# Kernel optimization log

Measured on AMD Instinct MI355X. Metric: run time of the kernel, lower is better.

The kernel has to match this reference:

```python
import jax, jax.numpy as jnp
import numpy as np

HID = 1024
DEPTH = 2

def _rhn_layer(x, Win, bin_, Wh, bh, Wt, bt):
    # x: [B, T, in]; returns outputs [B, T, H]
    B = x.shape[0]
    h0 = jnp.zeros((B, HID), dtype=x.dtype)
    xt = jnp.swapaxes(x, 0, 1)  # [T, B, in]

    def step(h_prev, x_t):
        h = x_t @ Win + bin_
        for i in range(DEPTH):
            t_gate = jax.nn.sigmoid(h @ Wt[i] + bt[i])
            h_layer = jnp.tanh(h @ Wh[i] + bh[i])
            h = t_gate * h_layer + (1.0 - t_gate) * h
        h_new = h + h_prev
        return h_new, h_new

    _, outs = jax.lax.scan(step, h0, xt)  # [T, B, H]
    return jnp.swapaxes(outs, 0, 1)


def setup_inputs() -> dict:
    key = jax.random.key(0)
    ks = jax.random.split(key, 16)
    B, T, IN, H, OUT = 64, 256, 128, HID, 128
    s = lambda fan_in: 1.0 / np.sqrt(fan_in)
    d = {}
    d["x"] = jax.random.normal(ks[0], (B, T, IN), dtype=jnp.float32)
    # layer 0 (input_size=IN)
    d["l0_Win"] = jax.random.uniform(ks[1], (IN, H), minval=-s(IN), maxval=s(IN))
    d["l0_bin"] = jax.random.uniform(ks[2], (H,), minval=-s(IN), maxval=s(IN))
    d["l0_Wh"] = jax.random.uniform(ks[3], (DEPTH, H, H), minval=-s(H), maxval=s(H))
    d["l0_bh"] = jax.random.uniform(ks[4], (DEPTH, H), minval=-s(H), maxval=s(H))
    d["l0_Wt"] = jax.random.uniform(ks[5], (DEPTH, H, H), minval=-s(H), maxval=s(H))
    d["l0_bt"] = jax.random.uniform(ks[6], (DEPTH, H), minval=-s(H), maxval=s(H))
    # layer 1 (input_size=H)
    d["l1_Win"] = jax.random.uniform(ks[7], (H, H), minval=-s(H), maxval=s(H))
    d["l1_bin"] = jax.random.uniform(ks[8], (H,), minval=-s(H), maxval=s(H))
    d["l1_Wh"] = jax.random.uniform(ks[9], (DEPTH, H, H), minval=-s(H), maxval=s(H))
    d["l1_bh"] = jax.random.uniform(ks[10], (DEPTH, H), minval=-s(H), maxval=s(H))
    d["l1_Wt"] = jax.random.uniform(ks[11], (DEPTH, H, H), minval=-s(H), maxval=s(H))
    d["l1_bt"] = jax.random.uniform(ks[12], (DEPTH, H), minval=-s(H), maxval=s(H))
    # final fc
    d["fc_W"] = jax.random.uniform(ks[13], (H, OUT), minval=-s(H), maxval=s(H))
    d["fc_b"] = jax.random.uniform(ks[14], (OUT,), minval=-s(H), maxval=s(H))
    return d


def reference(x, l0_Win, l0_bin, l0_Wh, l0_bh, l0_Wt, l0_bt,
              l1_Win, l1_bin, l1_Wh, l1_bh, l1_Wt, l1_bt, fc_W, fc_b):
    out = _rhn_layer(x, l0_Win, l0_bin, l0_Wh, l0_bh, l0_Wt, l0_bt)
    out = _rhn_layer(out, l1_Win, l1_bin, l1_Wh, l1_bh, l1_Wt, l1_bt)
    # forecast_horizon = 1 -> last time step only
    out = out[:, -1:, :] @ fc_W + fc_b  # [B, 1, OUT]
    return out
```

## Files before the change

### kernel.cpp

```cpp
#include <hip/hip_runtime.h>

typedef unsigned short u16;
typedef unsigned int u32;
typedef __bf16 bf16x8 __attribute__((ext_vector_type(8)));
typedef float floatx4 __attribute__((ext_vector_type(4)));

#define HID 1024
#define BATCH 64
#define SEQ 256
#define INDIM 128
#define OUTDIM 128
#define MROWS (BATCH*SEQ)
#define CUMP 140

__device__ __forceinline__ float b2f(u16 u) {
    union { u32 u; float f; } v; v.u = ((u32)u) << 16; return v.f;
}
__device__ __forceinline__ u16 f2b(float f) {
    union { float f; u32 u; } v; v.f = f;
    u32 x = v.u;
    x += 0x7fffu + ((x >> 16) & 1u);
    return (u16)(x >> 16);
}
__device__ __forceinline__ float sigm(float x) { return 1.f / (1.f + __expf(-x)); }
__device__ __forceinline__ float tanh_f(float x) { return 2.f / (1.f + __expf(-2.f * x)) - 1.f; }

__device__ __forceinline__ void gld16(const u16* g, u16* l) {
    __builtin_amdgcn_global_load_lds(
        (const __attribute__((address_space(1))) void*)g,
        (__attribute__((address_space(3))) void*)l, 16, 0, 0);
}

__device__ __forceinline__ void bar_sync() {
    asm volatile("" ::: "memory");
    __builtin_amdgcn_s_barrier();
    asm volatile("" ::: "memory");
}
template <int N>
__device__ __forceinline__ void vm_bar() {
    asm volatile("s_waitcnt vmcnt(%0)" :: "n"(N) : "memory");
    __builtin_amdgcn_s_barrier();
    asm volatile("" ::: "memory");
}

__device__ __forceinline__ int is_fp32(const u16* probe, int tid) {
    const int lane = tid & 63;
    const int e = (probe[lane * 7] >> 7) & 0xff;
    return __ballot(e >= 127) != 0ULL;
}

struct CvtList { const void* s[7]; u16* d[7]; int n[7]; };

__global__ void convert7(CvtList C, const u16* __restrict__ probe) {
    const int fp32 = is_fp32(probe, threadIdx.x);
    const int z = blockIdx.y;
    const int n = C.n[z];
    const int stride = gridDim.x * 256;
    for (int i = blockIdx.x * 256 + threadIdx.x; i < n; i += stride) {
        u16 o;
        if (fp32) o = f2b(((const float*)C.s[z])[i]);
        else      o = ((const u16*)C.s[z])[i];
        C.d[z][i] = o;
    }
}

struct TListO {
    const void* s[10];
    u16*        d[10];
    int         R[10];
    int         Cc[10];
    long        off[10];
};

__global__ void transpose10(TListO L, const u16* __restrict__ probe) {
    const int tx = threadIdx.x, ty = threadIdx.y;
    const int fp32 = is_fp32(probe, ty * 32 + tx);
    const int z = blockIdx.z;
    const void* src = L.s[z];
    u16*        dst = L.d[z];
    const int R  = L.R[z];
    const int Cc = L.Cc[z];
    const long zo = L.off[z];
    const int tr = blockIdx.y * 32, tc = blockIdx.x * 32;
    if (tr >= R || tc >= Cc) return;
    __align__(16) __shared__ u16 t[32][33];
#pragma unroll
    for (int i = 0; i < 4; ++i) {
        const int r = ty + i * 8;
        const long e = zo + (long)(tr + r) * Cc + tc + tx;
        u16 v;
        if (fp32) v = f2b(((const float*)src)[e]);
        else      v = ((const u16*)src)[e];
        t[r][tx] = v;
    }
    __syncthreads();
#pragma unroll
    for (int i = 0; i < 4; ++i) {
        const int r = ty + i * 8;
        dst[(size_t)(tc + r) * R + tr + tx] = t[tx][r];
    }
}

__device__ __forceinline__ void tile_swizzle(int& m0, int& n0) {
    const int lin = blockIdx.y * gridDim.x + blockIdx.x;
    const int xcd = lin & 7;
    const int loc = lin >> 3;
    m0 = (xcd * 16 + (loc & 15)) * 128;
    n0 = (loc >> 4) * 128;
}

__device__ __forceinline__ void tile_swizzle8(int& m0, int& n0) {
    const int lin = blockIdx.x;
    const int xcd = lin & 7;
    const int loc = lin >> 3;
    m0 = (xcd * 8 + (loc & 7)) * 256;
    n0 = (loc >> 3) * 128;
}

__global__ __launch_bounds__(256, 2) void gemm128(
    const u16* __restrict__ A, const u16* __restrict__ BT,
    const u16* __restrict__ bias, u16* __restrict__ C,
    int M, int N, int K)
{
    __align__(16) __shared__ u16 As[128 * 64];
    __align__(16) __shared__ u16 Bs[128 * 64];

    const int tid  = threadIdx.x;
    const int lane = tid & 63;
    const int wid  = tid >> 6;
    const int wr   = wid >> 1;
    const int wc   = wid & 1;

    int m0, n0;
    tile_swizzle(m0, n0);

    floatx4 acc[4][4] = {};

    const int srow = lane >> 3;
    const int scol = 8 * ((lane & 7) ^ (lane >> 3));
    const int cb   = wid * 4;
    const u16* Ag[4]; const u16* Bg[4];
    u16 *Al[4], *Bl[4];
#pragma unroll
    for (int j = 0; j < 4; ++j) {
        const int c = cb + j;
        const int r = c * 8 + srow;
        Ag[j] = A  + (size_t)(m0 + r) * K + scol;
        Bg[j] = BT + (size_t)(n0 + r) * K + scol;
        Al[j] = As + c * 512;
        Bl[j] = Bs + c * 512;
    }

    const int quad = lane >> 4;
    const int l16  = lane & 15;
    const int swz  = l16 & 7;

    const int nk = K >> 6;
    for (int kt = 0; kt < nk; ++kt) {
        __syncthreads();
#pragma unroll
        for (int j = 0; j < 4; ++j) {
            gld16(Ag[j], Al[j]);  gld16(Bg[j], Bl[j]);
            Ag[j] += 64; Bg[j] += 64;
        }
        __syncthreads();

#pragma unroll
        for (int kk = 0; kk < 2; ++kk) {
            const int slot = ((kk * 4 + quad) ^ swz) * 8;
            bf16x8 af[4], bfr[4];
#pragma unroll
            for (int i = 0; i < 4; ++i) {
                af[i]  = *(const bf16x8*)(As + (wr * 64 + i * 16 + l16) * 64 + slot);
                bfr[i] = *(const bf16x8*)(Bs + (wc * 64 + i * 16 + l16) * 64 + slot);
            }
#pragma unroll
            for (int i = 0; i < 4; ++i)
#pragma unroll
                for (int j = 0; j < 4; ++j)
                    acc[i][j] = __builtin_amdgcn_mfma_f32_16x16x32_bf16(af[i], bfr[j], acc[i][j], 0, 0, 0);
        }
    }

#pragma unroll
    for (int i = 0; i < 4; ++i) {
        const int rowb = m0 + wr * 64 + i * 16 + quad * 4;
#pragma unroll
        for (int j = 0; j < 4; ++j) {
            const int col = n0 + wc * 64 + j * 16 + l16;
            const float bv = b2f(bias[col]);
#pragma unroll
            for (int r = 0; r < 4; ++r)
                C[(size_t)(rowb + r) * N + col] = f2b(acc[i][j][r] + bv);
        }
    }
}

__global__ __launch_bounds__(256, 2) void gemm_hw(
    const u16* __restrict__ A,
    const u16* __restrict__ WtT,
    const u16* __restrict__ WhT,
    const u16* __restrict__ bt, const u16* __restrict__ bh,
    u16* __restrict__ Hout,
    int M, int N, int K)
{
    __align__(16) __shared__ u16 As [128 * 64];
    __align__(16) __shared__ u16 Bts[128 * 64];
    __align__(16) __shared__ u16 Bhs[128 * 64];

    const int tid  = threadIdx.x;
    const int lane = tid & 63;
    const int wid  = tid >> 6;
    const int wr   = wid >> 1;
    const int wc   = wid & 1;

    int m0, n0;
    tile_swizzle(m0, n0);

    floatx4 acct[4][4] = {};
    floatx4 acch[4][4] = {};

    const int srow = lane >> 3;
    const int scol = 8 * ((lane & 7) ^ (lane >> 3));
    const int cb   = wid * 4;
    const u16* Ag[4]; const u16* Tg[4]; const u16* Hg[4];
    u16 *Al[4], *Tl[4], *Hl[4];
#pragma unroll
    for (int j = 0; j < 4; ++j) {
        const int c = cb + j;
        const int r = c * 8 + srow;
        Ag[j] = A   + (size_t)(m0 + r) * K + scol;
        Tg[j] = WtT + (size_t)(n0 + r) * K + scol;
        Hg[j] = WhT + (size_t)(n0 + r) * K + scol;
        Al[j] = As  + c * 512;
        Tl[j] = Bts + c * 512;
        Hl[j] = Bhs + c * 512;
    }

    const int quad = lane >> 4;
    const int l16  = lane & 15;
    const int swz  = l16 & 7;

    const int nk = K >> 6;
    for (int kt = 0; kt < nk; ++kt) {
        __syncthreads();
#pragma unroll
        for (int j = 0; j < 4; ++j) {
            gld16(Ag[j], Al[j]);  gld16(Tg[j], Tl[j]);  gld16(Hg[j], Hl[j]);
            Ag[j] += 64; Tg[j] += 64; Hg[j] += 64;
        }
        __syncthreads();

#pragma unroll
        for (int kk = 0; kk < 2; ++kk) {
            const int slot = ((kk * 4 + quad) ^ swz) * 8;
            bf16x8 af[4], btf[4], bhf[4];
#pragma unroll
            for (int i = 0; i < 4; ++i) {
                af[i]  = *(const bf16x8*)(As  + (wr * 64 + i * 16 + l16) * 64 + slot);
                btf[i] = *(const bf16x8*)(Bts + (wc * 64 + i * 16 + l16) * 64 + slot);
                bhf[i] = *(const bf16x8*)(Bhs + (wc * 64 + i * 16 + l16) * 64 + slot);
            }
#pragma unroll
            for (int i = 0; i < 4; ++i)
#pragma unroll
                for (int j = 0; j < 4; ++j) {
                    acct[i][j] = __builtin_amdgcn_mfma_f32_16x16x32_bf16(af[i], btf[j], acct[i][j], 0, 0, 0);
                    acch[i][j] = __builtin_amdgcn_mfma_f32_16x16x32_bf16(af[i], bhf[j], acch[i][j], 0, 0, 0);
                }
        }
    }

#pragma unroll
    for (int i = 0; i < 4; ++i) {
        const int rowb = m0 + wr * 64 + i * 16 + quad * 4;
#pragma unroll
        for (int j = 0; j < 4; ++j) {
            const int col = n0 + wc * 64 + j * 16 + l16;
            const float btv = b2f(bt[col]);
            const float bhv = b2f(bh[col]);
#pragma unroll
            for (int r = 0; r < 4; ++r) {
                const size_t idx = (size_t)(rowb + r) * N + col;
                const float hold = b2f(A[idx]);
                const float tg = sigm(acct[i][j][r] + btv);
                const float hl = tanh_f(acch[i][j][r] + bhv);
                Hout[idx] = f2b(hold + tg * (hl - hold));
            }
        }
    }
}

__global__ __launch_bounds__(256, 2) void gemm_hw_sum(
    const u16* __restrict__ A,
    const u16* __restrict__ WtT,
    const u16* __restrict__ WhT,
    const u16* __restrict__ bt, const u16* __restrict__ bh,
    float* __restrict__ hpart,
    int M, int N, int K)
{
    __align__(16) __shared__ u16 As [128 * 64];
    __align__(16) __shared__ u16 Bts[128 * 64];
    __align__(16) __shared__ u16 Bhs[128 * 64];

    const int tid  = threadIdx.x;
    const int lane = tid & 63;
    const int wid  = tid >> 6;
    const int wr   = wid >> 1;
    const int wc   = wid & 1;

    int m0, n0;
    tile_swizzle(m0, n0);

    floatx4 acct[4][4] = {};
    floatx4 acch[4][4] = {};

    const int srow = lane >> 3;
    const int scol = 8 * ((lane & 7) ^ (lane >> 3));
    const int cb   = wid * 4;
    const u16* Ag[4]; const u16* Tg[4]; const u16* Hg[4];
    u16 *Al[4], *Tl[4], *Hl[4];
#pragma unroll
    for (int j = 0; j < 4; ++j) {
        const int c = cb + j;
        const int r = c * 8 + srow;
        Ag[j] = A   + (size_t)(m0 + r) * K + scol;
        Tg[j] = WtT + (size_t)(n0 + r) * K + scol;
        Hg[j] = WhT + (size_t)(n0 + r) * K + scol;
        Al[j] = As  + c * 512;
        Tl[j] = Bts + c * 512;
        Hl[j] = Bhs + c * 512;
    }

    const int quad = lane >> 4;
    const int l16  = lane & 15;
    const int swz  = l16 & 7;

    const int nk = K >> 6;
    for (int kt = 0; kt < nk; ++kt) {
        __syncthreads();
#pragma unroll
        for (int j = 0; j < 4; ++j) {
            gld16(Ag[j], Al[j]);  gld16(Tg[j], Tl[j]);  gld16(Hg[j], Hl[j]);
            Ag[j] += 64; Tg[j] += 64; Hg[j] += 64;
        }
        __syncthreads();

#pragma unroll
        for (int kk = 0; kk < 2; ++kk) {
            const int slot = ((kk * 4 + quad) ^ swz) * 8;
            bf16x8 af[4], btf[4], bhf[4];
#pragma unroll
            for (int i = 0; i < 4; ++i) {
                af[i]  = *(const bf16x8*)(As  + (wr * 64 + i * 16 + l16) * 64 + slot);
                btf[i] = *(const bf16x8*)(Bts + (wc * 64 + i * 16 + l16) * 64 + slot);
                bhf[i] = *(const bf16x8*)(Bhs + (wc * 64 + i * 16 + l16) * 64 + slot);
            }
#pragma unroll
            for (int i = 0; i < 4; ++i)
#pragma unroll
                for (int j = 0; j < 4; ++j) {
                    acct[i][j] = __builtin_amdgcn_mfma_f32_16x16x32_bf16(af[i], btf[j], acct[i][j], 0, 0, 0);
                    acch[i][j] = __builtin_amdgcn_mfma_f32_16x16x32_bf16(af[i], bhf[j], acch[i][j], 0, 0, 0);
                }
        }
    }

    const int b    = m0 >> 8;
    const int slot = ((m0 >> 7) & 1) * 2 + wr;
#pragma unroll
    for (int j = 0; j < 4; ++j) {
        const int col = n0 + wc * 64 + j * 16 + l16;
        const float btv = b2f(bt[col]);
        const float bhv = b2f(bh[col]);
        float colsum = 0.f;
#pragma unroll
        for (int i = 0; i < 4; ++i) {
            const int rowb = m0 + wr * 64 + i * 16 + quad * 4;
#pragma unroll
            for (int r = 0; r < 4; ++r) {
                const size_t idx = (size_t)(rowb + r) * N + col;
                const float hold = b2f(A[idx]);
                const float tg = sigm(acct[i][j][r] + btv);
                const float hl = tanh_f(acch[i][j][r] + bhv);
                colsum += hold + tg * (hl - hold);
            }
        }
        colsum += __shfl_xor(colsum, 16, 64);
        colsum += __shfl_xor(colsum, 32, 64);
        if (quad == 0)
            hpart[((size_t)(slot * BATCH + b)) * HID + col] = colsum;
    }
}

__device__ __forceinline__ void hw8_mainloop(
    u16* lds,
    const u16* __restrict__ A, const u16* __restrict__ WtT, const u16* __restrict__ WhT,
    int m0, int n0, int K,
    floatx4 (&acct)[4][4], floatx4 (&acch)[4][4])
{
    const int tid  = threadIdx.x;
    const int lane = tid & 63;
    const int wid  = tid >> 6;
    const int wr   = wid >> 1;
    const int wc   = wid & 1;

    const int srow = lane >> 3;
    const int scol = 8 * ((lane & 7) ^ srow);

    const u16* Ag = A   + (size_t)(m0 + wid * 32 + srow) * K + scol;
    const u16* Tg = WtT + (size_t)(n0 + wid * 16 + srow) * K + scol;
    const u16* Hg = WhT + (size_t)(n0 + wid * 16 + srow) * K + scol;
    const size_t K8 = (size_t)K * 8;

    u16* dA = lds + wid * 2048;
    u16* dT = lds + 16384 + wid * 1024;
    u16* dH = lds + 24576 + wid * 1024;

    const int quad = lane >> 4;
    const int l16  = lane & 15;
    const int swz  = l16 & 7;
    const int s0 = (quad ^ swz) * 8;
    const int s1 = ((4 + quad) ^ swz) * 8;
    const int ra = wr * 64 + l16;
    const int rb = wc * 64 + l16;

    gld16(Tg,           dT);
    gld16(Tg +     K8,  dT + 512);
    gld16(Ag,           dA);
    gld16(Ag +     K8,  dA + 512);
    gld16(Ag + 2 * K8,  dA + 1024);
    gld16(Ag + 3 * K8,  dA + 1536);
    gld16(Hg,           dH);
    gld16(Hg +     K8,  dH + 512);
    Ag += 64; Tg += 64; Hg += 64;
    vm_bar<2>();

    const int nk = K >> 6;
    for (int kt = 0; kt < nk; ++kt) {
        const int  cur = kt & 1;
        const int  nb  = (cur ^ 1) * 32768;
        const bool pf  = (kt + 1 < nk);
        const u16* Sa = lds + cur * 32768;
        const u16* St = Sa + 16384;
        const u16* Sh = Sa + 24576;

        bf16x8 af0[4], af1[4], bq[4];

#pragma unroll
        for (int i = 0; i < 4; ++i) {
            af0[i] = *(const bf16x8*)(Sa + (ra + i * 16) * 64 + s0);
            bq[i]  = *(const bf16x8*)(St + (rb + i * 16) * 64 + s0);
        }
        if (pf) {
            gld16(Tg,      dT + nb);  gld16(Tg + K8, dT + nb + 512);
            gld16(Ag,      dA + nb);  gld16(Ag + K8, dA + nb + 512);
        }
        bar_sync();
        __builtin_amdgcn_s_setprio(1);
#pragma unroll
        for (int i = 0; i < 4; ++i)
#pragma unroll
            for (int j = 0; j < 4; ++j)
                acct[i][j] = __builtin_amdgcn_mfma_f32_16x16x32_bf16(af0[i], bq[j], acct[i][j], 0, 0, 0);
        __builtin_amdgcn_s_setprio(0);

#pragma unroll
        for (int i = 0; i < 4; ++i) {
            af1[i] = *(const bf16x8*)(Sa + (ra + i * 16) * 64 + s1);
            bq[i]  = *(const bf16x8*)(St + (rb + i * 16) * 64 + s1);
        }
        if (pf) {
            gld16(Ag + 2 * K8, dA + nb + 1024);
            gld16(Ag + 3 * K8, dA + nb + 1536);
            vm_bar<6>();
        } else {
            vm_bar<0>();
        }
        __builtin_amdgcn_s_setprio(1);
#pragma unroll
        for (int i = 0; i < 4; ++i)
#pragma unroll
            for (int j = 0; j < 4; ++j)
                acct[i][j] = __builtin_amdgcn_mfma_f32_16x16x32_bf16(af1[i], bq[j], acct[i][j], 0, 0, 0);
        __builtin_amdgcn_s_setprio(0);

#pragma unroll
        for (int i = 0; i < 4; ++i)
            bq[i] = *(const bf16x8*)(Sh + (rb + i * 16) * 64 + s0);
        bar_sync();
        __builtin_amdgcn_s_setprio(1);
#pragma unroll
        for (int i = 0; i < 4; ++i)
#pragma unroll
            for (int j = 0; j < 4; ++j)
                acch[i][j] = __builtin_amdgcn_mfma_f32_16x16x32_bf16(af0[i], bq[j], acch[i][j], 0, 0, 0);
        __builtin_amdgcn_s_setprio(0);

#pragma unroll
        for (int i = 0; i < 4; ++i)
            bq[i] = *(const bf16x8*)(Sh + (rb + i * 16) * 64 + s1);
        if (pf) {
            gld16(Hg,      dH + nb);
            gld16(Hg + K8, dH + nb + 512);
            vm_bar<2>();
        } else {
            bar_sync();
        }
        __builtin_amdgcn_s_setprio(1);
#pragma unroll
        for (int i = 0; i < 4; ++i)
#pragma unroll
            for (int j = 0; j < 4; ++j)
                acch[i][j] = __builtin_amdgcn_mfma_f32_16x16x32_bf16(af1[i], bq[j], acch[i][j], 0, 0, 0);
        __builtin_amdgcn_s_setprio(0);

        Ag += 64; Tg += 64; Hg += 64;
    }
}

__global__ __launch_bounds__(512, 2) void gemm_hw8_cum(
    const u16* __restrict__ A,
    const u16* __restrict__ WtT,
    const u16* __restrict__ WhT,
    const u16* __restrict__ bt, const u16* __restrict__ bh,
    u16* __restrict__ Y,
    int M, int N, int K)
{
    __align__(16) __shared__ u16 lds[65536];
    __shared__ float tot[512];

    int m0, n0;
    tile_swizzle8(m0, n0);

    floatx4 acct[4][4] = {};
    floatx4 acch[4][4] = {};
    hw8_mainloop(lds, A, WtT, WhT, m0, n0, K, acct, acch);

    const int tid  = threadIdx.x;
    const int lane = tid & 63;
    const int wid  = tid >> 6;
    const int wr   = wid >> 1;
    const int wc   = wid & 1;
    const int quad = lane >> 4;
    const int l16  = lane & 15;

    __syncthreads();

#pragma unroll
    for (int i = 0; i < 4; ++i) {
        const int rowl = wr * 64 + i * 16 + quad * 4;
#pragma unroll
        for (int j = 0; j < 4; ++j) {
            const int coll = wc * 64 + j * 16 + l16;
            const float btv = b2f(bt[n0 + coll]);
            const float bhv = b2f(bh[n0 + coll]);
#pragma unroll
            for (int r = 0; r < 4; ++r) {
                const size_t idx = (size_t)(m0 + rowl + r) * N + n0 + coll;
                const float hold = b2f(A[idx]);
                const float tg = sigm(acct[i][j][r] + btv);
                const float hl = tanh_f(acch[i][j][r] + bhv);
                lds[(rowl + r) * CUMP + coll] = f2b(hold + tg * (hl - hold));
            }
        }
    }
    __syncthreads();

    const int seg  = tid >> 7;
    const int colc = tid & 127;
    const int base = seg * 64 * CUMP + colc;
    {
        float local = 0.f;
#pragma unroll 8
        for (int t = 0; t < 64; ++t)
            local += b2f(lds[base + t * CUMP]);
        tot[seg * 128 + colc] = local;
    }
    __syncthreads();
    {
        float off = 0.f;
#pragma unroll
        for (int s = 0; s < 3; ++s)
            off += (s < seg) ? tot[s * 128 + colc] : 0.f;
        float acc = off;
#pragma unroll 8
        for (int t = 0; t < 64; ++t) {
            const int o = base + t * CUMP;
            acc += b2f(lds[o]);
            lds[o] = f2b(acc);
        }
    }
    __syncthreads();

#pragma unroll
    for (int it = 0; it < 16; ++it) {
        const int o   = it * 2048 + tid * 4;
        const int row = o >> 7;
        const int col = o & 127;
        *(uint2*)&Y[(size_t)(m0 + row) * N + n0 + col] =
            *(const uint2*)&lds[row * CUMP + col];
    }
}

__global__ void fc_final(const float* __restrict__ hp, const void* __restrict__ W,
                         const void* __restrict__ bias, void* __restrict__ out) {
    __shared__ float sh[HID];
    const int fp32 = is_fp32((const u16*)W, threadIdx.x);
    const int b = blockIdx.x, o = threadIdx.x;
    for (int k = o; k < HID; k += 128) {
        float v = 0.f;
#pragma unroll
        for (int s = 0; s < 4; ++s)
            v += hp[((size_t)(s * BATCH + b)) * HID + k];
        sh[k] = v;
    }
    __syncthreads();
    float acc;
    if (fp32) {
        acc = ((const float*)bias)[o];
        for (int k = 0; k < HID; ++k)
            acc += sh[k] * ((const float*)W)[(size_t)k * OUTDIM + o];
        ((float*)out)[b * OUTDIM + o] = acc;
    } else {
        acc = b2f(((const u16*)bias)[o]);
        for (int k = 0; k < HID; ++k)
            acc += sh[k] * b2f(((const u16*)W)[(size_t)k * OUTDIM + o]);
        ((u16*)out)[b * OUTDIM + o] = f2b(acc);
    }
}

extern "C" void kernel_launch(void* const* d_in, const int* in_sizes, int n_in,
                              void* d_out, int out_size, void* d_ws, size_t ws_size,
                              hipStream_t stream) {
    const void* x      = d_in[0];
    const void* l0_Win = d_in[1];
    const void* l0_bin = d_in[2];
    const void* l0_Wh  = d_in[3];
    const void* l0_bh  = d_in[4];
    const void* l0_Wt  = d_in[5];
    const void* l0_bt  = d_in[6];
    const void* l1_Win = d_in[7];
    const void* l1_bin = d_in[8];
    const void* l1_Wh  = d_in[9];
    const void* l1_bh  = d_in[10];
    const void* l1_Wt  = d_in[11];
    const void* l1_bt  = d_in[12];
    const void* fc_W   = d_in[13];
    const void* fc_b   = d_in[14];

    char* ws = (char*)d_ws;
    u16* Pa = (u16*)(ws);
    u16* Pb = (u16*)(ws + 33554432);
    u16* xc = Pb;
    u16* tW = (u16*)(ws + 67108864);
    u16* tWin0 = tW;
    u16* tWt00 = tWin0 + 131072;
    u16* tWt01 = tWt00 + 1048576;
    u16* tWh00 = tWt01 + 1048576;
    u16* tWh01 = tWh00 + 1048576;
    u16* tWin1 = tWh01 + 1048576;
    u16* tWt10 = tWin1 + 1048576;
    u16* tWt11 = tWt10 + 1048576;
    u16* tWh10 = tWt11 + 1048576;
    u16* tWh11 = tWh10 + 1048576;
    u16* smallb = tWh11 + 1048576;
    u16* binc0 = smallb;
    u16* bhc0  = binc0 + 1024;
    u16* btc0  = bhc0 + 2048;
    u16* binc1 = btc0 + 2048;
    u16* bhc1  = binc1 + 1024;
    u16* btc1  = bhc1 + 2048;
    float* hpart = (float*)Pb;

    const u16* probe = (const u16*)l0_Wh;

    const long DD = (long)HID * HID;
    TListO L;
    L.s[0] = l0_Win; L.d[0] = tWin0; L.R[0] = INDIM; L.Cc[0] = HID; L.off[0] = 0;
    L.s[1] = l0_Wt;  L.d[1] = tWt00; L.R[1] = HID;   L.Cc[1] = HID; L.off[1] = 0;
    L.s[2] = l0_Wt;  L.d[2] = tWt01; L.R[2] = HID;   L.Cc[2] = HID; L.off[2] = DD;
    L.s[3] = l0_Wh;  L.d[3] = tWh00; L.R[3] = HID;   L.Cc[3] = HID; L.off[3] = 0;
    L.s[4] = l0_Wh;  L.d[4] = tWh01; L.R[4] = HID;   L.Cc[4] = HID; L.off[4] = DD;
    L.s[5] = l1_Win; L.d[5] = tWin1; L.R[5] = HID;   L.Cc[5] = HID; L.off[5] = 0;
    L.s[6] = l1_Wt;  L.d[6] = tWt10; L.R[6] = HID;   L.Cc[6] = HID; L.off[6] = 0;
    L.s[7] = l1_Wt;  L.d[7] = tWt11; L.R[7] = HID;   L.Cc[7] = HID; L.off[7] = DD;
    L.s[8] = l1_Wh;  L.d[8] = tWh10; L.R[8] = HID;   L.Cc[8] = HID; L.off[8] = 0;
    L.s[9] = l1_Wh;  L.d[9] = tWh11; L.R[9] = HID;   L.Cc[9] = HID; L.off[9] = DD;
    transpose10<<<dim3(32, 32, 10), dim3(32, 8), 0, stream>>>(L, probe);

    CvtList C7;
    C7.s[0] = x;      C7.d[0] = xc;    C7.n[0] = MROWS * INDIM;
    C7.s[1] = l0_bin; C7.d[1] = binc0; C7.n[1] = HID;
    C7.s[2] = l0_bh;  C7.d[2] = bhc0;  C7.n[2] = 2 * HID;
    C7.s[3] = l0_bt;  C7.d[3] = btc0;  C7.n[3] = 2 * HID;
    C7.s[4] = l1_bin; C7.d[4] = binc1; C7.n[4] = HID;
    C7.s[5] = l1_bh;  C7.d[5] = bhc1;  C7.n[5] = 2 * HID;
    C7.s[6] = l1_bt;  C7.d[6] = btc1;  C7.n[6] = 2 * HID;
    convert7<<<dim3(512, 7), 256, 0, stream>>>(C7, probe);

    gemm128<<<dim3(8, 128), 256, 0, stream>>>(xc, tWin0, binc0, Pa, MROWS, HID, INDIM);
    gemm_hw<<<dim3(8, 128), 256, 0, stream>>>(Pa, tWt00, tWh00, btc0, bhc0, Pb, MROWS, HID, HID);
    gemm_hw8_cum<<<512, 512, 0, stream>>>(Pb, tWt01, tWh01, btc0 + HID, bhc0 + HID, Pa, MROWS, HID, HID);

    gemm128<<<dim3(8, 128), 256, 0, stream>>>(Pa, tWin1, binc1, Pb, MROWS, HID, HID);
    gemm_hw<<<dim3(8, 128), 256, 0, stream>>>(Pb, tWt10, tWh10, btc1, bhc1, Pa, MROWS, HID, HID);
    gemm_hw_sum<<<dim3(8, 128), 256, 0, stream>>>(Pa, tWt11, tWh11, btc1 + HID, bhc1 + HID,
                                                  hpart, MROWS, HID, HID);

    fc_final<<<64, 128, 0, stream>>>(hpart, fc_W, fc_b, d_out);
}
```

Baseline: 520.0 us.

## Fold layer-0 input projection into first highway gate weights

Precomputes Win0·Wt00 and Win0·Wh00 (with folded biases) so the first highway sublayer of layer 0 runs directly from the 128-wide input instead of the 1024-wide projected hidden state. This replaces the K=1024 gate GEMM with a K=128 fused kernel that computes the projection, both gates and the highway combine in one pass, and removes the intermediate write and read of the projected activations. The cost is two small prep kernels each call. Rounding the folded weights to bf16 changes numerics slightly.

Measured after the change: 505.5 us. 1.03x faster.

```diff
diff --git a/kernel.cpp b/kernel.cpp
--- a/kernel.cpp
+++ b/kernel.cpp
@@ -49,9 +49,9 @@
     return __ballot(e >= 127) != 0ULL;
 }
 
-struct CvtList { const void* s[7]; u16* d[7]; int n[7]; };
-
-__global__ void convert7(CvtList C, const u16* __restrict__ probe) {
+struct CvtList { const void* s[8]; u16* d[8]; int n[8]; };
+
+__global__ void convert8(CvtList C, const u16* __restrict__ probe) {
     const int fp32 = is_fp32(probe, threadIdx.x);
     const int z = blockIdx.y;
     const int n = C.n[z];
@@ -192,6 +192,211 @@
 #pragma unroll
             for (int r = 0; r < 4; ++r)
                 C[(size_t)(rowb + r) * N + col] = f2b(acc[i][j][r] + bv);
+        }
+    }
+}
+
+__global__ __launch_bounds__(256, 2) void gemm_wp(
+    const u16* __restrict__ At, const u16* __restrict__ Ah,
+    const u16* __restrict__ BT, u16* __restrict__ Ct, u16* __restrict__ Ch)
+{
+    const u16* A = blockIdx.y ? Ah : At;
+    u16*       C = blockIdx.y ? Ch : Ct;
+    const int m0 = blockIdx.x * 128;
+    const int K = HID, N = 128;
+
+    __align__(16) __shared__ u16 As[128 * 64];
+    __align__(16) __shared__ u16 Bs[128 * 64];
+
+    const int tid  = threadIdx.x;
+    const int lane = tid & 63;
+    const int wid  = tid >> 6;
+    const int wr   = wid >> 1;
+    const int wc   = wid & 1;
+
+    floatx4 acc[4][4] = {};
+
+    const int srow = lane >> 3;
+    const int scol = 8 * ((lane & 7) ^ (lane >> 3));
+    const int cb   = wid * 4;
+    const u16* Ag[4]; const u16* Bg[4];
+    u16 *Al[4], *Bl[4];
+#pragma unroll
+    for (int j = 0; j < 4; ++j) {
+        const int c = cb + j;
+        const int r = c * 8 + srow;
+        Ag[j] = A  + (size_t)(m0 + r) * K + scol;
+        Bg[j] = BT + (size_t)r * K + scol;
+        Al[j] = As + c * 512;
+        Bl[j] = Bs + c * 512;
+    }
+
+    const int quad = lane >> 4;
+    const int l16  = lane & 15;
+    const int swz  = l16 & 7;
+
+    for (int kt = 0; kt < (K >> 6); ++kt) {
+        __syncthreads();
+#pragma unroll
+        for (int j = 0; j < 4; ++j) {
+            gld16(Ag[j], Al[j]);  gld16(Bg[j], Bl[j]);
+            Ag[j] += 64; Bg[j] += 64;
+        }
+        __syncthreads();
+
+#pragma unroll
+        for (int kk = 0; kk < 2; ++kk) {
+            const int slot = ((kk * 4 + quad) ^ swz) * 8;
+            bf16x8 af[4], bfr[4];
+#pragma unroll
+            for (int i = 0; i < 4; ++i) {
+                af[i]  = *(const bf16x8*)(As + (wr * 64 + i * 16 + l16) * 64 + slot);
+                bfr[i] = *(const bf16x8*)(Bs + (wc * 64 + i * 16 + l16) * 64 + slot);
+            }
+#pragma unroll
+            for (int i = 0; i < 4; ++i)
+#pragma unroll
+                for (int j = 0; j < 4; ++j)
+                    acc[i][j] = __builtin_amdgcn_mfma_f32_16x16x32_bf16(af[i], bfr[j], acc[i][j], 0, 0, 0);
+        }
+    }
+
+#pragma unroll
+    for (int i = 0; i < 4; ++i) {
+        const int rowb = m0 + wr * 64 + i * 16 + quad * 4;
+#pragma unroll
+        for (int j = 0; j < 4; ++j) {
+            const int col = wc * 64 + j * 16 + l16;
+#pragma unroll
+            for (int r = 0; r < 4; ++r)
+                C[(size_t)(rowb + r) * N + col] = f2b(acc[i][j][r]);
+        }
+    }
+}
+
+__global__ void bias_fold(const u16* __restrict__ tWt, const u16* __restrict__ tWh,
+                          const u16* __restrict__ binv, const u16* __restrict__ bt0,
+                          const u16* __restrict__ bh0,
+                          u16* __restrict__ obt, u16* __restrict__ obh)
+{
+    const u16* tW = blockIdx.y ? tWh : tWt;
+    const u16* bo = blockIdx.y ? bh0 : bt0;
+    u16*       ob = blockIdx.y ? obh : obt;
+    const int j = blockIdx.x * 128 + threadIdx.x;
+    const u16* row = tW + (size_t)j * HID;
+    float acc = 0.f;
+    for (int k = 0; k < HID; k += 8) {
+        uint4 wv = *(const uint4*)(row + k);
+        uint4 bv = *(const uint4*)(binv + k);
+        const u16* w = (const u16*)&wv;
+        const u16* b = (const u16*)&bv;
+#pragma unroll
+        for (int e = 0; e < 8; ++e) acc += b2f(b[e]) * b2f(w[e]);
+    }
+    ob[j] = f2b(acc + b2f(bo[j]));
+}
+
+__global__ __launch_bounds__(512, 2) void gemm_hw3(
+    const u16* __restrict__ A,
+    const u16* __restrict__ WtP,
+    const u16* __restrict__ WhP,
+    const u16* __restrict__ WiT,
+    const u16* __restrict__ bpt, const u16* __restrict__ bph,
+    const u16* __restrict__ bin,
+    u16* __restrict__ Hout,
+    int M, int N, int K)
+{
+    __align__(16) __shared__ u16 As [128 * 64];
+    __align__(16) __shared__ u16 Bts[128 * 64];
+    __align__(16) __shared__ u16 Bhs[128 * 64];
+    __align__(16) __shared__ u16 Bis[128 * 64];
+
+    const int tid  = threadIdx.x;
+    const int lane = tid & 63;
+    const int wid  = tid >> 6;
+    const int wm   = wid >> 2;
+    const int wn   = wid & 3;
+
+    int m0, n0;
+    tile_swizzle(m0, n0);
+
+    floatx4 acct[4][2] = {};
+    floatx4 acch[4][2] = {};
+    floatx4 acci[4][2] = {};
+
+    const int srow = lane >> 3;
+    const int scol = 8 * ((lane & 7) ^ srow);
+    const u16* Ag[2]; const u16* Tg[2]; const u16* Hg[2]; const u16* Ig[2];
+    u16 *Al[2], *Tl[2], *Hl[2], *Il[2];
+#pragma unroll
+    for (int j = 0; j < 2; ++j) {
+        const int c = wid * 2 + j;
+        const int r = c * 8 + srow;
+        Ag[j] = A   + (size_t)(m0 + r) * K + scol;
+        Tg[j] = WtP + (size_t)(n0 + r) * K + scol;
+        Hg[j] = WhP + (size_t)(n0 + r) * K + scol;
+        Ig[j] = WiT + (size_t)(n0 + r) * K + scol;
+        Al[j] = As  + c * 512;
+        Tl[j] = Bts + c * 512;
+        Hl[j] = Bhs + c * 512;
+        Il[j] = Bis + c * 512;
+    }
+
+    const int quad = lane >> 4;
+    const int l16  = lane & 15;
+    const int swz  = l16 & 7;
+
+    const int nk = K >> 6;
+    for (int kt = 0; kt < nk; ++kt) {
+        __syncthreads();
+#pragma unroll
+        for (int j = 0; j < 2; ++j) {
+            gld16(Ag[j], Al[j]);  gld16(Tg[j], Tl[j]);
+            gld16(Hg[j], Hl[j]);  gld16(Ig[j], Il[j]);
+            Ag[j] += 64; Tg[j] += 64; Hg[j] += 64; Ig[j] += 64;
+        }
+        __syncthreads();
+
+#pragma unroll
+        for (int kk = 0; kk < 2; ++kk) {
+            const int slot = ((kk * 4 + quad) ^ swz) * 8;
+            bf16x8 af[4], btf[2], bhf[2], bif[2];
+#pragma unroll
+            for (int i = 0; i < 4; ++i)
+                af[i] = *(const bf16x8*)(As + (wm * 64 + i * 16 + l16) * 64 + slot);
+#pragma unroll
+            for (int j = 0; j < 2; ++j) {
+                btf[j] = *(const bf16x8*)(Bts + (wn * 32 + j * 16 + l16) * 64 + slot);
+                bhf[j] = *(const bf16x8*)(Bhs + (wn * 32 + j * 16 + l16) * 64 + slot);
+                bif[j] = *(const bf16x8*)(Bis + (wn * 32 + j * 16 + l16) * 64 + slot);
+            }
+#pragma unroll
+            for (int i = 0; i < 4; ++i)
+#pragma unroll
+                for (int j = 0; j < 2; ++j) {
+                    acct[i][j] = __builtin_amdgcn_mfma_f32_16x16x32_bf16(af[i], btf[j], acct[i][j], 0, 0, 0);
+                    acch[i][j] = __builtin_amdgcn_mfma_f32_16x16x32_bf16(af[i], bhf[j], acch[i][j], 0, 0, 0);
+                    acci[i][j] = __builtin_amdgcn_mfma_f32_16x16x32_bf16(af[i], bif[j], acci[i][j], 0, 0, 0);
+                }
+        }
+    }
+
+#pragma unroll
+    for (int i = 0; i < 4; ++i) {
+        const int rowb = m0 + wm * 64 + i * 16 + quad * 4;
+#pragma unroll
+        for (int j = 0; j < 2; ++j) {
+            const int col = n0 + wn * 32 + j * 16 + l16;
+            const float biv = b2f(bin[col]);
+            const float btv = b2f(bpt[col]);
+            const float bhv = b2f(bph[col]);
+#pragma unroll
+            for (int r = 0; r < 4; ++r) {
+                const float h  = acci[i][j][r] + biv;
+                const float tg = sigm(acct[i][j][r] + btv);
+                const float hl = tanh_f(acch[i][j][r] + bhv);
+                Hout[(size_t)(rowb + r) * N + col] = f2b(h + tg * (hl - h));
+            }
         }
     }
 }
@@ -671,7 +876,12 @@
     u16* binc1 = btc0 + 2048;
     u16* bhc1  = binc1 + 1024;
     u16* btc1  = bhc1 + 2048;
-    float* hpart = (float*)Pb;
+    u16* Win0c = btc1 + 2048;
+    u16* Wpt   = Win0c + 131072;
+    u16* Wph   = Wpt + 131072;
+    u16* bpt   = Wph + 131072;
+    u16* bph   = bpt + 1024;
+    float* hpart = (float*)Pa;
 
     const u16* probe = (const u16*)l0_Wh;
 
@@ -689,23 +899,27 @@
     L.s[9] = l1_Wh;  L.d[9] = tWh11; L.R[9] = HID;   L.Cc[9] = HID; L.off[9] = DD;
     transpose10<<<dim3(32, 32, 10), dim3(32, 8), 0, stream>>>(L, probe);
 
-    CvtList C7;
-    C7.s[0] = x;      C7.d[0] = xc;    C7.n[0] = MROWS * INDIM;
-    C7.s[1] = l0_bin; C7.d[1] = binc0; C7.n[1] = HID;
-    C7.s[2] = l0_bh;  C7.d[2] = bhc0;  C7.n[2] = 2 * HID;
-    C7.s[3] = l0_bt;  C7.d[3] = btc0;  C7.n[3] = 2 * HID;
-    C7.s[4] = l1_bin; C7.d[4] = binc1; C7.n[4] = HID;
-    C7.s[5] = l1_bh;  C7.d[5] = bhc1;  C7.n[5] = 2 * HID;
-    C7.s[6] = l1_bt;  C7.d[6] = btc1;  C7.n[6] = 2 * HID;
-    convert7<<<dim3(512, 7), 256, 0, stream>>>(C7, probe);
-
-    gemm128<<<dim3(8, 128), 256, 0, stream>>>(xc, tWin0, binc0, Pa, MROWS, HID, INDIM);
-    gemm_hw<<<dim3(8, 128), 256, 0, stream>>>(Pa, tWt00, tWh00, btc0, bhc0, Pb, MROWS, HID, HID);
-    gemm_hw8_cum<<<512, 512, 0, stream>>>(Pb, tWt01, tWh01, btc0 + HID, bhc0 + HID, Pa, MROWS, HID, HID);
-
-    gemm128<<<dim3(8, 128), 256, 0, stream>>>(Pa, tWin1, binc1, Pb, MROWS, HID, HID);
-    gemm_hw<<<dim3(8, 128), 256, 0, stream>>>(Pb, tWt10, tWh10, btc1, bhc1, Pa, MROWS, HID, HID);
-    gemm_hw_sum<<<dim3(8, 128), 256, 0, stream>>>(Pa, tWt11, tWh11, btc1 + HID, bhc1 + HID,
+    CvtList C8;
+    C8.s[0] = x;      C8.d[0] = xc;    C8.n[0] = MROWS * INDIM;
+    C8.s[1] = l0_bin; C8.d[1] = binc0; C8.n[1] = HID;
+    C8.s[2] = l0_bh;  C8.d[2] = bhc0;  C8.n[2] = 2 * HID;
+    C8.s[3] = l0_bt;  C8.d[3] = btc0;  C8.n[3] = 2 * HID;
+    C8.s[4] = l1_bin; C8.d[4] = binc1; C8.n[4] = HID;
+    C8.s[5] = l1_bh;  C8.d[5] = bhc1;  C8.n[5] = 2 * HID;
+    C8.s[6] = l1_bt;  C8.d[6] = btc1;  C8.n[6] = 2 * HID;
+    C8.s[7] = l0_Win; C8.d[7] = Win0c; C8.n[7] = INDIM * HID;
+    convert8<<<dim3(512, 8), 256, 0, stream>>>(C8, probe);
+
+    gemm_wp<<<dim3(8, 2), 256, 0, stream>>>(tWt00, tWh00, Win0c, Wpt, Wph);
+    bias_fold<<<dim3(8, 2), 128, 0, stream>>>(tWt00, tWh00, binc0, btc0, bhc0, bpt, bph);
+
+    gemm_hw3<<<dim3(8, 128), 512, 0, stream>>>(xc, Wpt, Wph, tWin0, bpt, bph, binc0,
+                                               Pa, MROWS, HID, INDIM);
+    gemm_hw8_cum<<<512, 512, 0, stream>>>(Pa, tWt01, tWh01, btc0 + HID, bhc0 + HID, Pb, MROWS, HID, HID);
+
+    gemm128<<<dim3(8, 128), 256, 0, stream>>>(Pb, tWin1, binc1, Pa, MROWS, HID, HID);
+    gemm_hw<<<dim3(8, 128), 256, 0, stream>>>(Pa, tWt10, tWh10, btc1, bhc1, Pb, MROWS, HID, HID);
+    gemm_hw_sum<<<dim3(8, 128), 256, 0, stream>>>(Pb, tWt11, tWh11, btc1 + HID, bhc1 + HID,
                                                   hpart, MROWS, HID, HID);
 
     fc_final<<<64, 128, 0, stream>>>(hpart, fc_W, fc_b, d_out);
```
